# Kernel optimization log

Measured on AMD Instinct MI355X. Metric: run time of the kernel, lower is better.

The kernel has to match this reference:

```python
import jax, jax.numpy as jnp
import numpy as np


def setup_inputs() -> dict:
    key = jax.random.key(0)
    k1, k2 = jax.random.split(key)
    B, C, h, w = 8, 128, 56, 56
    query_feature = jax.random.normal(k1, (B, C, h, w), dtype=jnp.float32)
    support_feature = jax.random.normal(k2, (B, C, h, w), dtype=jnp.float32)
    return {"query_feature": query_feature, "support_feature": support_feature}


def reference(query_feature, support_feature):
    q, s = query_feature, support_feature
    B, C, h, w = support_feature.shape
    N = h * w
    # torch .view semantics == row-major reshape (NOT a transpose)
    qf = jnp.reshape(query_feature, (B, N, C))      # [B, N, C]
    sf = jnp.reshape(support_feature, (B, C, N))    # [B, C, N]
    batch_adj = jnp.einsum('bnc,bcm->bnm', qf, sf)  # [B, N, N]
    attn = jax.nn.softmax(batch_adj, axis=-1)
    query_logits = jnp.einsum('bnm,bmc->bnc', attn, qf)          # [B, N, C]
    attention_mask = jax.nn.sigmoid(jnp.sum(batch_adj, axis=-1)) # [B, N]
    query_logits = query_logits * attention_mask[..., None]
    sf2 = jnp.reshape(support_feature, (B, N, C))   # another raw view
    support_logits = sf2 * attention_mask[..., None]
    query_logits = jnp.reshape(query_logits, (B, C, h, w))
    support_logits = jnp.reshape(support_logits, (B, C, h, w))
    return (q + query_logits, s + support_logits)
```

## Files before the change

kernel.cpp:

```cpp
#include <hip/hip_runtime.h>
#include <math.h>

#define B_ 8
#define C_ 128
#define N_ 3136
#define MT 64
#define QTBIG 128
#define TILES 49
#define QTILES 25
#define SPLIT0 25

typedef short bf16x8 __attribute__((ext_vector_type(8)));
typedef float f32x4 __attribute__((ext_vector_type(4)));

__device__ __forceinline__ unsigned short f2bf(float f) {
    union { float f; unsigned u; } x; x.f = f;
    return (unsigned short)((x.u + 0x8000u) >> 16);
}

__device__ __forceinline__ void gl_lds16(const void* g, void* l) {
    __builtin_amdgcn_global_load_lds(
        (const __attribute__((address_space(1))) unsigned int*)g,
        (__attribute__((address_space(3))) unsigned int*)l, 16, 0, 0);
}

__global__ __launch_bounds__(256) void colsum_kernel(const float* __restrict__ s,
                                                     float* __restrict__ csum) {
    int blk = blockIdx.x;
    const float* p = s + (size_t)blk * N_;
    float acc = 0.f;
    for (int i = threadIdx.x; i < N_; i += 256) acc += p[i];
#pragma unroll
    for (int off = 32; off > 0; off >>= 1) acc += __shfl_down(acc, off, 64);
    __shared__ float part[4];
    if ((threadIdx.x & 63) == 0) part[threadIdx.x >> 6] = acc;
    __syncthreads();
    if (threadIdx.x == 0) csum[blk] = part[0] + part[1] + part[2] + part[3];
}

__global__ __launch_bounds__(256) void prep_kernel(const float* __restrict__ q,
                                                   const float* __restrict__ s,
                                                   unsigned short* __restrict__ sfT,
                                                   unsigned short* __restrict__ qfT) {
    __shared__ unsigned short T[8448];
    const int tid = threadIdx.x, bid = blockIdx.x;
    const int b = bid & 7, m0 = (bid >> 3) * 64;
    const float* sb = s + (size_t)b * C_ * N_;
    const float* qb = q + (size_t)b * C_ * N_;

    unsigned short (*TA)[132] = (unsigned short (*)[132])T;
#pragma unroll
    for (int st = 0; st < 8; ++st) {
        int idx = st * 256 + tid;
        int c = idx >> 4, m4 = (idx & 15) * 4;
        float4 v = *(const float4*)&sb[(size_t)c * N_ + m0 + m4];
        TA[m4 + 0][c] = f2bf(v.x);
        TA[m4 + 1][c] = f2bf(v.y);
        TA[m4 + 2][c] = f2bf(v.z);
        TA[m4 + 3][c] = f2bf(v.w);
    }
    __syncthreads();
    {
        unsigned short* dst = sfT + (size_t)b * N_ * C_;
#pragma unroll
        for (int st = 0; st < 4; ++st) {
            int g = st * 256 + tid;
            int mr = g >> 4, p = g & 15;
            int lch = p ^ (mr & 15);
            const unsigned short* src = &TA[mr][lch * 8];
            ushort4 a = *(const ushort4*)src;
            ushort4 bq = *(const ushort4*)(src + 4);
            uint4 w;
            w.x = a.x | ((unsigned)a.y << 16);   w.y = a.z | ((unsigned)a.w << 16);
            w.z = bq.x | ((unsigned)bq.y << 16); w.w = bq.z | ((unsigned)bq.w << 16);
            *(uint4*)&dst[(size_t)(m0 + mr) * C_ + p * 8] = w;
        }
    }
    __syncthreads();

    unsigned short (*TB)[66] = (unsigned short (*)[66])T;
#pragma unroll
    for (int st = 0; st < 8; ++st) {
        int idx = st * 256 + tid;
        int r = idx >> 5, c4 = (idx & 31) * 4;
        float4 v = *(const float4*)&qb[(size_t)(m0 + r) * C_ + c4];
        TB[c4 + 0][r] = f2bf(v.x);
        TB[c4 + 1][r] = f2bf(v.y);
        TB[c4 + 2][r] = f2bf(v.z);
        TB[c4 + 3][r] = f2bf(v.w);
    }
    __syncthreads();
    {
        unsigned short* dst = qfT + (size_t)b * C_ * N_;
#pragma unroll
        for (int st = 0; st < 4; ++st) {
            int g = st * 256 + tid;
            int c = g >> 3, p = g & 7;
            int lch = p ^ (c & 7);
            const unsigned short* src = &TB[c][lch * 8];
            ushort2 a0 = *(const ushort2*)(src);
            ushort2 a1 = *(const ushort2*)(src + 2);
            ushort2 a2 = *(const ushort2*)(src + 4);
            ushort2 a3 = *(const ushort2*)(src + 6);
            uint4 w;
            w.x = a0.x | ((unsigned)a0.y << 16); w.y = a1.x | ((unsigned)a1.y << 16);
            w.z = a2.x | ((unsigned)a2.y << 16); w.w = a3.x | ((unsigned)a3.y << 16);
            *(uint4*)&dst[(size_t)c * N_ + m0 + p * 8] = w;
        }
    }
}

__global__ __launch_bounds__(256, 2) void fused_split_kernel(
    const float* __restrict__ q,
    const unsigned short* __restrict__ sfT,
    const unsigned short* __restrict__ qfT,
    float* __restrict__ Opart, float* __restrict__ dpart) {

    __shared__ __align__(16) unsigned short Kb[2][MT * C_];
    __shared__ __align__(16) unsigned short Vb[2][C_ * MT];

    const int tid = threadIdx.x;
    const int lane = tid & 63;
    const int wave = tid >> 6;
    const int l15 = lane & 15;
    const int quad = lane >> 4;
    const int bid = blockIdx.x;
    const int b = bid & 7;
    const int rest = bid >> 3;
    const int qt = rest % QTILES;
    const int split = rest / QTILES;
    const int n0 = qt * QTBIG;
    const int t0 = split ? SPLIT0 : 0;
    const int t1 = split ? TILES : SPLIT0;

    const float* qb = q + (size_t)b * C_ * N_;
    const unsigned short* sfTb = sfT + (size_t)b * N_ * C_;
    const unsigned short* qfTb = qfT + (size_t)b * C_ * N_;

    const int sig_base = ((l15 >> 2) << 3) + (l15 & 3);

    {
        const size_t m1 = (size_t)t0 * MT;
#pragma unroll
        for (int st = 0; st < 4; ++st) {
            int i = st * 256 + tid;
            gl_lds16(sfTb + (m1 + (i >> 4)) * C_ + (i & 15) * 8,
                     &Kb[0][(st * 256 + wave * 64) * 8]);
            gl_lds16(qfTb + (size_t)(i >> 3) * N_ + m1 + (i & 7) * 8,
                     &Vb[0][(st * 256 + wave * 64) * 8]);
        }
    }

    bf16x8 qa[2][4];
#pragma unroll
    for (int rt = 0; rt < 2; ++rt) {
        int grow = n0 + wave * 32 + rt * 16 + l15;
        if (grow > N_ - 1) grow = N_ - 1;
#pragma unroll
        for (int ks = 0; ks < 4; ++ks) {
            int c0 = ks * 32 + quad * 8;
            float4 f0 = *(const float4*)&qb[(size_t)grow * C_ + c0];
            float4 f1 = *(const float4*)&qb[(size_t)grow * C_ + c0 + 4];
            union { unsigned short u[8]; bf16x8 v; } t;
            t.u[0] = f2bf(f0.x); t.u[1] = f2bf(f0.y);
            t.u[2] = f2bf(f0.z); t.u[3] = f2bf(f0.w);
            t.u[4] = f2bf(f1.x); t.u[5] = f2bf(f1.y);
            t.u[6] = f2bf(f1.z); t.u[7] = f2bf(f1.w);
            qa[rt][ks] = t.v;
        }
    }

    f32x4 O[2][8];
#pragma unroll
    for (int rt = 0; rt < 2; ++rt)
#pragma unroll
        for (int nt = 0; nt < 8; ++nt) O[rt][nt] = (f32x4){0.f, 0.f, 0.f, 0.f};
    float dsum[2] = {0.f, 0.f};

    const int ntiles = t1 - t0;
    for (int tt = 0; tt < ntiles; ++tt) {
        const int cur = tt & 1;
        __syncthreads();

        if (tt + 1 < ntiles) {
            const int nxt = cur ^ 1;
            const size_t m1 = (size_t)(t0 + tt + 1) * MT;
#pragma unroll
            for (int st = 0; st < 4; ++st) {
                int i = st * 256 + tid;
                gl_lds16(sfTb + (m1 + (i >> 4)) * C_ + (i & 15) * 8,
                         &Kb[nxt][(st * 256 + wave * 64) * 8]);
                gl_lds16(qfTb + (size_t)(i >> 3) * N_ + m1 + (i & 7) * 8,
                         &Vb[nxt][(st * 256 + wave * 64) * 8]);
            }
        }

        f32x4 acc[4][2];
#pragma unroll
        for (int ct = 0; ct < 4; ++ct) {
            acc[ct][0] = (f32x4){0.f, 0.f, 0.f, 0.f};
            acc[ct][1] = (f32x4){0.f, 0.f, 0.f, 0.f};
            const int mrow = sig_base + ((ct & 1) << 2) + ((ct >> 1) << 5);
#pragma unroll
            for (int ks = 0; ks < 4; ++ks) {
                int ch = (ks * 4 + quad) ^ (mrow & 15);
                bf16x8 af = *(const bf16x8*)&Kb[cur][mrow * C_ + ch * 8];
                acc[ct][0] = __builtin_amdgcn_mfma_f32_16x16x32_bf16(af, qa[0][ks], acc[ct][0], 0, 0, 0);
                acc[ct][1] = __builtin_amdgcn_mfma_f32_16x16x32_bf16(af, qa[1][ks], acc[ct][1], 0, 0, 0);
            }
        }

        bf16x8 pa[2][2];
#pragma unroll
        for (int k2 = 0; k2 < 2; ++k2)
#pragma unroll
            for (int rt = 0; rt < 2; ++rt) {
                float e0 = __expf(acc[2 * k2 + 0][rt][0]);
                float e1 = __expf(acc[2 * k2 + 0][rt][1]);
                float e2 = __expf(acc[2 * k2 + 0][rt][2]);
                float e3 = __expf(acc[2 * k2 + 0][rt][3]);
                float e4 = __expf(acc[2 * k2 + 1][rt][0]);
                float e5 = __expf(acc[2 * k2 + 1][rt][1]);
                float e6 = __expf(acc[2 * k2 + 1][rt][2]);
                float e7 = __expf(acc[2 * k2 + 1][rt][3]);
                dsum[rt] += ((e0 + e1) + (e2 + e3)) + ((e4 + e5) + (e6 + e7));
                union { unsigned short u[8]; bf16x8 v; } pk;
                pk.u[0] = f2bf(e0); pk.u[1] = f2bf(e1);
                pk.u[2] = f2bf(e2); pk.u[3] = f2bf(e3);
                pk.u[4] = f2bf(e4); pk.u[5] = f2bf(e5);
                pk.u[6] = f2bf(e6); pk.u[7] = f2bf(e7);
                pa[rt][k2] = pk.v;
            }

#pragma unroll
        for (int k2 = 0; k2 < 2; ++k2)
#pragma unroll
            for (int nt = 0; nt < 8; ++nt) {
                const int crow = nt * 16 + l15;
                int ch = (k2 * 4 + quad) ^ (crow & 7);
                bf16x8 vf = *(const bf16x8*)&Vb[cur][crow * MT + ch * 8];
                O[0][nt] = __builtin_amdgcn_mfma_f32_16x16x32_bf16(pa[0][k2], vf, O[0][nt], 0, 0, 0);
                O[1][nt] = __builtin_amdgcn_mfma_f32_16x16x32_bf16(pa[1][k2], vf, O[1][nt], 0, 0, 0);
            }
    }

#pragma unroll
    for (int rt = 0; rt < 2; ++rt) {
        float d = dsum[rt];
        d += __shfl_xor(d, 16, 64);
        d += __shfl_xor(d, 32, 64);
        if (quad == 0) {
            int grow = n0 + wave * 32 + rt * 16 + l15;
            if (grow < N_)
                dpart[(size_t)(split * 8 + b) * N_ + grow] = d;
        }
    }

#pragma unroll
    for (int rt = 0; rt < 2; ++rt)
#pragma unroll
        for (int r = 0; r < 4; ++r) {
            int grow = n0 + wave * 32 + rt * 16 + quad * 4 + r;
            if (grow < N_) {
                float* dst = Opart + ((size_t)(split * 8 + b) * N_ + grow) * C_;
#pragma unroll
                for (int nt = 0; nt < 8; ++nt)
                    dst[nt * 16 + l15] = O[rt][nt][r];
            }
        }
}

__global__ __launch_bounds__(256) void combine_kernel(
    const float* __restrict__ q, const float* __restrict__ s,
    const float* __restrict__ csum, const float* __restrict__ Opart,
    const float* __restrict__ dpart,
    float* __restrict__ out0, float* __restrict__ out1) {

    __shared__ float cs[C_];
    const int tid = threadIdx.x, bid = blockIdx.x;
    const int b = bid & 7, r0 = (bid >> 3) * 32;
    if (tid < C_) cs[tid] = csum[b * C_ + tid];
    __syncthreads();

    const int lane = tid & 63, wave = tid >> 6;
    const int row_l = wave * 8 + (lane >> 3);
    const int j = lane & 7;
    const int grow = r0 + row_l;
    const size_t base = (size_t)b * N_ * C_ + (size_t)grow * C_;

    float4 qv[4];
    float dot = 0.f;
#pragma unroll
    for (int k = 0; k < 4; ++k) {
        int c = k * 32 + j * 4;
        qv[k] = *(const float4*)&q[base + c];
        dot += qv[k].x * cs[c] + qv[k].y * cs[c + 1] +
               qv[k].z * cs[c + 2] + qv[k].w * cs[c + 3];
    }
    dot += __shfl_xor(dot, 1, 64);
    dot += __shfl_xor(dot, 2, 64);
    dot += __shfl_xor(dot, 4, 64);
    const float mask = 1.0f / (1.0f + __expf(-dot));

    const float dtot = dpart[(size_t)b * N_ + grow] +
                       dpart[(size_t)(8 + b) * N_ + grow];
    const float scl = mask / dtot;
    const float om = 1.0f + mask;

    const size_t p0 = ((size_t)b * N_ + grow) * C_;
    const size_t p1 = p0 + (size_t)8 * N_ * C_;
#pragma unroll
    for (int k = 0; k < 4; ++k) {
        int c = k * 32 + j * 4;
        float4 oa = *(const float4*)&Opart[p0 + c];
        float4 ob = *(const float4*)&Opart[p1 + c];
        float4 sv = *(const float4*)&s[base + c];
        float4 r0v, r1v;
        r0v.x = qv[k].x + (oa.x + ob.x) * scl;
        r0v.y = qv[k].y + (oa.y + ob.y) * scl;
        r0v.z = qv[k].z + (oa.z + ob.z) * scl;
        r0v.w = qv[k].w + (oa.w + ob.w) * scl;
        r1v.x = sv.x * om; r1v.y = sv.y * om;
        r1v.z = sv.z * om; r1v.w = sv.w * om;
        *(float4*)&out0[base + c] = r0v;
        *(float4*)&out1[base + c] = r1v;
    }
}

__global__ __launch_bounds__(256, 2) void fused_kernel(const float* __restrict__ q,
                                                       const float* __restrict__ s,
                                                       const float* __restrict__ csum,
                                                       float* __restrict__ out0,
                                                       float* __restrict__ out1) {
    __shared__ float QtT[C_][68];
    __shared__ float Kt[C_ * 32];
    __shared__ float Vt[32 * C_];
    __shared__ float PT[32][68];
    __shared__ float mask_l[64];
    __shared__ float csum_l[C_];

    const int t = threadIdx.x;
    const int l = t & 63, w = t >> 6, tx = t & 15, ty = t >> 4;
    const int bid = blockIdx.x, b = bid & 7, n0 = (bid >> 3) * 64;
    const float* qb = q + (size_t)b * C_ * N_;
    const float* sb = s + (size_t)b * C_ * N_;

#pragma unroll
    for (int jj = 0; jj < 2; ++jj) {
        int c = l + 64 * jj;
#pragma unroll
        for (int i = 0; i < 16; ++i) QtT[c][w + 4 * i] = qb[(size_t)(n0 + w + 4 * i) * C_ + c];
    }
    if (t < C_) csum_l[t] = csum[b * C_ + t];
    __syncthreads();
    if (t < 64) {
        float d = 0.f;
        for (int c = 0; c < C_; ++c) d += QtT[c][t] * csum_l[c];
        mask_l[t] = 1.0f / (1.0f + __expf(-d));
    }
    float4 Oa[4], Ob[4];
#pragma unroll
    for (int i = 0; i < 4; ++i) { Oa[i] = make_float4(0,0,0,0); Ob[i] = make_float4(0,0,0,0); }
    float m_r[4], l_r[4];
#pragma unroll
    for (int i = 0; i < 4; ++i) { m_r[i] = -3.0e38f; l_r[i] = 0.f; }

    for (int mt = 0; mt < N_ / 32; ++mt) {
        const int m0 = mt * 32;
        __syncthreads();
#pragma unroll
        for (int i = 0; i < 4; ++i) {
            int s4 = (w * 4 + i) * 64 + l;
            int c = s4 >> 3, mq = (s4 & 7) * 4;
            *(float4*)&Kt[c * 32 + mq] = *(const float4*)&sb[(size_t)c * N_ + m0 + mq];
            *(float4*)&Vt[s4 * 4] = *(const float4*)&qb[(size_t)m0 * C_ + s4 * 4];
        }
        __syncthreads();
        float a[4][2];
#pragma unroll
        for (int i = 0; i < 4; ++i) a[i][0] = a[i][1] = 0.f;
#pragma unroll 4
        for (int k = 0; k < C_; ++k) {
            const float4 qv = *(const float4*)&QtT[k][4 * ty];
            const float2 kv = *(const float2*)&Kt[k * 32 + 2 * tx];
            a[0][0] = fmaf(qv.x, kv.x, a[0][0]); a[0][1] = fmaf(qv.x, kv.y, a[0][1]);
            a[1][0] = fmaf(qv.y, kv.x, a[1][0]); a[1][1] = fmaf(qv.y, kv.y, a[1][1]);
            a[2][0] = fmaf(qv.z, kv.x, a[2][0]); a[2][1] = fmaf(qv.z, kv.y, a[2][1]);
            a[3][0] = fmaf(qv.w, kv.x, a[3][0]); a[3][1] = fmaf(qv.w, kv.y, a[3][1]);
        }
#pragma unroll
        for (int i = 0; i < 4; ++i) {
            float tm = fmaxf(a[i][0], a[i][1]);
            tm = fmaxf(tm, __shfl_xor(tm, 1, 64)); tm = fmaxf(tm, __shfl_xor(tm, 2, 64));
            tm = fmaxf(tm, __shfl_xor(tm, 4, 64)); tm = fmaxf(tm, __shfl_xor(tm, 8, 64));
            float nm = fmaxf(m_r[i], tm);
            float al = __expf(m_r[i] - nm);
            m_r[i] = nm;
            float p0 = __expf(a[i][0] - nm), p1 = __expf(a[i][1] - nm);
            float ts = p0 + p1;
            ts += __shfl_xor(ts, 1, 64); ts += __shfl_xor(ts, 2, 64);
            ts += __shfl_xor(ts, 4, 64); ts += __shfl_xor(ts, 8, 64);
            l_r[i] = l_r[i] * al + ts;
            PT[2 * tx + 0][4 * ty + i] = p0;
            PT[2 * tx + 1][4 * ty + i] = p1;
            Oa[i].x *= al; Oa[i].y *= al; Oa[i].z *= al; Oa[i].w *= al;
            Ob[i].x *= al; Ob[i].y *= al; Ob[i].z *= al; Ob[i].w *= al;
        }
        __syncthreads();
#pragma unroll 2
        for (int j = 0; j < 32; ++j) {
            const float4 pv = *(const float4*)&PT[j][4 * ty];
            const float4 v0 = *(const float4*)&Vt[j * C_ + 4 * tx];
            const float4 v1 = *(const float4*)&Vt[j * C_ + 4 * tx + 64];
            Oa[0].x = fmaf(pv.x, v0.x, Oa[0].x); Oa[0].y = fmaf(pv.x, v0.y, Oa[0].y);
            Oa[0].z = fmaf(pv.x, v0.z, Oa[0].z); Oa[0].w = fmaf(pv.x, v0.w, Oa[0].w);
            Ob[0].x = fmaf(pv.x, v1.x, Ob[0].x); Ob[0].y = fmaf(pv.x, v1.y, Ob[0].y);
            Ob[0].z = fmaf(pv.x, v1.z, Ob[0].z); Ob[0].w = fmaf(pv.x, v1.w, Ob[0].w);
            Oa[1].x = fmaf(pv.y, v0.x, Oa[1].x); Oa[1].y = fmaf(pv.y, v0.y, Oa[1].y);
            Oa[1].z = fmaf(pv.y, v0.z, Oa[1].z); Oa[1].w = fmaf(pv.y, v0.w, Oa[1].w);
            Ob[1].x = fmaf(pv.y, v1.x, Ob[1].x); Ob[1].y = fmaf(pv.y, v1.y, Ob[1].y);
            Ob[1].z = fmaf(pv.y, v1.z, Ob[1].z); Ob[1].w = fmaf(pv.y, v1.w, Ob[1].w);
            Oa[2].x = fmaf(pv.z, v0.x, Oa[2].x); Oa[2].y = fmaf(pv.z, v0.y, Oa[2].y);
            Oa[2].z = fmaf(pv.z, v0.z, Oa[2].z); Oa[2].w = fmaf(pv.z, v0.w, Oa[2].w);
            Ob[2].x = fmaf(pv.z, v1.x, Ob[2].x); Ob[2].y = fmaf(pv.z, v1.y, Ob[2].y);
            Ob[2].z = fmaf(pv.z, v1.z, Ob[2].z); Ob[2].w = fmaf(pv.z, v1.w, Ob[2].w);
            Oa[3].x = fmaf(pv.w, v0.x, Oa[3].x); Oa[3].y = fmaf(pv.w, v0.y, Oa[3].y);
            Oa[3].z = fmaf(pv.w, v0.z, Oa[3].z); Oa[3].w = fmaf(pv.w, v0.w, Oa[3].w);
            Ob[3].x = fmaf(pv.w, v1.x, Ob[3].x); Ob[3].y = fmaf(pv.w, v1.y, Ob[3].y);
            Ob[3].z = fmaf(pv.w, v1.z, Ob[3].z); Ob[3].w = fmaf(pv.w, v1.w, Ob[3].w);
        }
    }
#pragma unroll
    for (int i = 0; i < 4; ++i) {
        const int r = 4 * ty + i;
        const float mk = mask_l[r];
        const float scl = mk / l_r[i];
        const float om = 1.0f + mk;
        const size_t row = (size_t)b * C_ * N_ + (size_t)(n0 + r) * C_;
#pragma unroll
        for (int h = 0; h < 2; ++h) {
            const int c = 4 * tx + 64 * h;
            const float4 ov = h ? Ob[i] : Oa[i];
            float4 qv = *(const float4*)&qb[(size_t)(n0 + r) * C_ + c];
            float4 sv = *(const float4*)&sb[(size_t)(n0 + r) * C_ + c];
            float4 o0, o1;
            o0.x = qv.x + ov.x * scl; o0.y = qv.y + ov.y * scl;
            o0.z = qv.z + ov.z * scl; o0.w = qv.w + ov.w * scl;
            o1.x = sv.x * om; o1.y = sv.y * om; o1.z = sv.z * om; o1.w = sv.w * om;
            *(float4*)&out0[row + c] = o0;
            *(float4*)&out1[row + c] = o1;
        }
    }
}

extern "C" void kernel_launch(void* const* d_in, const int* in_sizes, int n_in,
                              void* d_out, int out_size, void* d_ws, size_t ws_size,
                              hipStream_t stream) {
    const float* q = (const float*)d_in[0];
    const float* s = (const float*)d_in[1];
    float* out0 = (float*)d_out;
    float* out1 = out0 + (size_t)B_ * C_ * N_;
    float* csum = (float*)d_ws;

    const size_t elems = (size_t)B_ * N_ * C_;
    const size_t need = 4096
                      + 2 * elems * sizeof(unsigned short)
                      + 2 * elems * sizeof(float)
                      + 2 * (size_t)B_ * N_ * sizeof(float);

    colsum_kernel<<<B_ * C_, 256, 0, stream>>>(s, csum);
    if (ws_size >= need) {
        unsigned short* sfT = (unsigned short*)((char*)d_ws + 4096);
        unsigned short* qfT = sfT + elems;
        float* Opart = (float*)(qfT + elems);
        float* dpart = Opart + 2 * elems;
        prep_kernel<<<B_ * TILES, 256, 0, stream>>>(q, s, sfT, qfT);
        fused_split_kernel<<<2 * QTILES * B_, 256, 0, stream>>>(q, sfT, qfT, Opart, dpart);
        combine_kernel<<<B_ * (N_ / 32), 256, 0, stream>>>(q, s, csum, Opart, dpart, out0, out1);
    } else {
        fused_kernel<<<B_ * (N_ / 64), 256, 0, stream>>>(q, s, csum, out0, out1);
    }
}
```

Measured before the change: 149.0 us.

## Split key range four ways, fuse colsum into prep, register-stage V buffer

Generalizes the key-dimension split from 2 to a runtime nsplit (4 when the workspace allows), giving 800 blocks instead of 400 for better CU fill. The separate colsum kernel is replaced by atomic partial sums inside prep_kernel after a memset. V is now single-buffered in LDS and prefetched through registers, which frees LDS so occupancy can rise to 3 blocks per SM. The costs are more partial-output traffic in the combine kernel, an extra barrier per tile, and float atomics that make the column sums nondeterministic in order.

After: 303.6 us. +103.7%, slower.

```diff
diff --git a/kernel.cpp b/kernel.cpp
--- a/kernel.cpp
+++ b/kernel.cpp
@@ -8,7 +8,6 @@
 #define QTBIG 128
 #define TILES 49
 #define QTILES 25
-#define SPLIT0 25
 
 typedef short bf16x8 __attribute__((ext_vector_type(8)));
 typedef float f32x4 __attribute__((ext_vector_type(4)));
@@ -41,7 +40,8 @@
 __global__ __launch_bounds__(256) void prep_kernel(const float* __restrict__ q,
                                                    const float* __restrict__ s,
                                                    unsigned short* __restrict__ sfT,
-                                                   unsigned short* __restrict__ qfT) {
+                                                   unsigned short* __restrict__ qfT,
+                                                   float* __restrict__ csum) {
     __shared__ unsigned short T[8448];
     const int tid = threadIdx.x, bid = blockIdx.x;
     const int b = bid & 7, m0 = (bid >> 3) * 64;
@@ -58,6 +58,12 @@
         TA[m4 + 1][c] = f2bf(v.y);
         TA[m4 + 2][c] = f2bf(v.z);
         TA[m4 + 3][c] = f2bf(v.w);
+        float part = v.x + v.y + v.z + v.w;
+        part += __shfl_xor(part, 1, 64);
+        part += __shfl_xor(part, 2, 64);
+        part += __shfl_xor(part, 4, 64);
+        part += __shfl_xor(part, 8, 64);
+        if ((tid & 15) == 0) atomicAdd(&csum[b * C_ + c], part);
     }
     __syncthreads();
     {
@@ -110,14 +116,15 @@
     }
 }
 
-__global__ __launch_bounds__(256, 2) void fused_split_kernel(
+__global__ __launch_bounds__(256, 3) void fused_split_kernel(
     const float* __restrict__ q,
     const unsigned short* __restrict__ sfT,
     const unsigned short* __restrict__ qfT,
-    float* __restrict__ Opart, float* __restrict__ dpart) {
+    float* __restrict__ Opart, float* __restrict__ dpart,
+    int nsplit) {
 
     __shared__ __align__(16) unsigned short Kb[2][MT * C_];
-    __shared__ __align__(16) unsigned short Vb[2][C_ * MT];
+    __shared__ __align__(16) unsigned short Vb[C_ * MT];
 
     const int tid = threadIdx.x;
     const int lane = tid & 63;
@@ -130,8 +137,9 @@
     const int qt = rest % QTILES;
     const int split = rest / QTILES;
     const int n0 = qt * QTBIG;
-    const int t0 = split ? SPLIT0 : 0;
-    const int t1 = split ? TILES : SPLIT0;
+    const int per = TILES / nsplit, rem = TILES % nsplit;
+    const int t0 = split * per + (split < rem ? split : rem);
+    const int ntiles = per + (split < rem ? 1 : 0);
 
     const float* qb = q + (size_t)b * C_ * N_;
     const unsigned short* sfTb = sfT + (size_t)b * N_ * C_;
@@ -147,7 +155,7 @@
             gl_lds16(sfTb + (m1 + (i >> 4)) * C_ + (i & 15) * 8,
                      &Kb[0][(st * 256 + wave * 64) * 8]);
             gl_lds16(qfTb + (size_t)(i >> 3) * N_ + m1 + (i & 7) * 8,
-                     &Vb[0][(st * 256 + wave * 64) * 8]);
+                     &Vb[(st * 256 + wave * 64) * 8]);
         }
     }
 
@@ -177,12 +185,12 @@
         for (int nt = 0; nt < 8; ++nt) O[rt][nt] = (f32x4){0.f, 0.f, 0.f, 0.f};
     float dsum[2] = {0.f, 0.f};
 
-    const int ntiles = t1 - t0;
     for (int tt = 0; tt < ntiles; ++tt) {
         const int cur = tt & 1;
+        const int more = (tt + 1 < ntiles);
         __syncthreads();
 
-        if (tt + 1 < ntiles) {
+        if (more) {
             const int nxt = cur ^ 1;
             const size_t m1 = (size_t)(t0 + tt + 1) * MT;
 #pragma unroll
@@ -190,8 +198,6 @@
                 int i = st * 256 + tid;
                 gl_lds16(sfTb + (m1 + (i >> 4)) * C_ + (i & 15) * 8,
                          &Kb[nxt][(st * 256 + wave * 64) * 8]);
-                gl_lds16(qfTb + (size_t)(i >> 3) * N_ + m1 + (i & 7) * 8,
-                         &Vb[nxt][(st * 256 + wave * 64) * 8]);
             }
         }
 
@@ -232,16 +238,35 @@
                 pa[rt][k2] = pk.v;
             }
 
+        uint4 vreg[4];
+        if (more) {
+            const size_t m1 = (size_t)(t0 + tt + 1) * MT;
+#pragma unroll
+            for (int j = 0; j < 4; ++j) {
+                int i = j * 256 + tid;
+                vreg[j] = *(const uint4*)(qfTb + (size_t)(i >> 3) * N_ + m1 + (i & 7) * 8);
+            }
+        }
+
 #pragma unroll
         for (int k2 = 0; k2 < 2; ++k2)
 #pragma unroll
             for (int nt = 0; nt < 8; ++nt) {
                 const int crow = nt * 16 + l15;
                 int ch = (k2 * 4 + quad) ^ (crow & 7);
-                bf16x8 vf = *(const bf16x8*)&Vb[cur][crow * MT + ch * 8];
+                bf16x8 vf = *(const bf16x8*)&Vb[crow * MT + ch * 8];
                 O[0][nt] = __builtin_amdgcn_mfma_f32_16x16x32_bf16(pa[0][k2], vf, O[0][nt], 0, 0, 0);
                 O[1][nt] = __builtin_amdgcn_mfma_f32_16x16x32_bf16(pa[1][k2], vf, O[1][nt], 0, 0, 0);
             }
+
+        if (more) {
+            __syncthreads();
+#pragma unroll
+            for (int j = 0; j < 4; ++j) {
+                int i = j * 256 + tid;
+                *(uint4*)&Vb[i * 8] = vreg[j];
+            }
+        }
     }
 
 #pragma unroll
@@ -274,7 +299,7 @@
     const float* __restrict__ q, const float* __restrict__ s,
     const float* __restrict__ csum, const float* __restrict__ Opart,
     const float* __restrict__ dpart,
-    float* __restrict__ out0, float* __restrict__ out1) {
+    float* __restrict__ out0, float* __restrict__ out1, int nsplit) {
 
     __shared__ float cs[C_];
     const int tid = threadIdx.x, bid = blockIdx.x;
@@ -302,24 +327,27 @@
     dot += __shfl_xor(dot, 4, 64);
     const float mask = 1.0f / (1.0f + __expf(-dot));
 
-    const float dtot = dpart[(size_t)b * N_ + grow] +
-                       dpart[(size_t)(8 + b) * N_ + grow];
+    float dtot = 0.f;
+    for (int sp = 0; sp < nsplit; ++sp)
+        dtot += dpart[(size_t)(sp * 8 + b) * N_ + grow];
     const float scl = mask / dtot;
     const float om = 1.0f + mask;
 
-    const size_t p0 = ((size_t)b * N_ + grow) * C_;
-    const size_t p1 = p0 + (size_t)8 * N_ * C_;
 #pragma unroll
     for (int k = 0; k < 4; ++k) {
         int c = k * 32 + j * 4;
-        float4 oa = *(const float4*)&Opart[p0 + c];
-        float4 ob = *(const float4*)&Opart[p1 + c];
+        float4 oa = make_float4(0.f, 0.f, 0.f, 0.f);
+        for (int sp = 0; sp < nsplit; ++sp) {
+            const size_t p = ((size_t)(sp * 8 + b) * N_ + grow) * C_;
+            float4 t = *(const float4*)&Opart[p + c];
+            oa.x += t.x; oa.y += t.y; oa.z += t.z; oa.w += t.w;
+        }
         float4 sv = *(const float4*)&s[base + c];
         float4 r0v, r1v;
-        r0v.x = qv[k].x + (oa.x + ob.x) * scl;
-        r0v.y = qv[k].y + (oa.y + ob.y) * scl;
-        r0v.z = qv[k].z + (oa.z + ob.z) * scl;
-        r0v.w = qv[k].w + (oa.w + ob.w) * scl;
+        r0v.x = qv[k].x + oa.x * scl;
+        r0v.y = qv[k].y + oa.y * scl;
+        r0v.z = qv[k].z + oa.z * scl;
+        r0v.w = qv[k].w + oa.w * scl;
         r1v.x = sv.x * om; r1v.y = sv.y * om;
         r1v.z = sv.z * om; r1v.w = sv.w * om;
         *(float4*)&out0[base + c] = r0v;
@@ -463,21 +491,30 @@
     float* csum = (float*)d_ws;
 
     const size_t elems = (size_t)B_ * N_ * C_;
-    const size_t need = 4096
-                      + 2 * elems * sizeof(unsigned short)
-                      + 2 * elems * sizeof(float)
-                      + 2 * (size_t)B_ * N_ * sizeof(float);
-
-    colsum_kernel<<<B_ * C_, 256, 0, stream>>>(s, csum);
-    if (ws_size >= need) {
+    auto need = [&](int ns) {
+        return (size_t)4096
+             + 2 * elems * sizeof(unsigned short)
+             + (size_t)ns * elems * sizeof(float)
+             + (size_t)ns * B_ * N_ * sizeof(float);
+    };
+
+    int ns = 0;
+    if (ws_size >= need(4)) ns = 4;
+    else if (ws_size >= need(2)) ns = 2;
+
+    if (ns > 0) {
         unsigned short* sfT = (unsigned short*)((char*)d_ws + 4096);
         unsigned short* qfT = sfT + elems;
         float* Opart = (float*)(qfT + elems);
-        float* dpart = Opart + 2 * elems;
-        prep_kernel<<<B_ * TILES, 256, 0, stream>>>(q, s, sfT, qfT);
-        fused_split_kernel<<<2 * QTILES * B_, 256, 0, stream>>>(q, sfT, qfT, Opart, dpart);
-        combine_kernel<<<B_ * (N_ / 32), 256, 0, stream>>>(q, s, csum, Opart, dpart, out0, out1);
+        float* dpart = Opart + (size_t)ns * elems;
+        hipMemsetAsync(csum, 0, B_ * C_ * sizeof(float), stream);
+        prep_kernel<<<B_ * TILES, 256, 0, stream>>>(q, s, sfT, qfT, csum);
+        fused_split_kernel<<<ns * QTILES * B_, 256, 0, stream>>>(
+            q, sfT, qfT, Opart, dpart, ns);
+        combine_kernel<<<B_ * (N_ / 32), 256, 0, stream>>>(q, s, csum, Opart, dpart,
+                                                           out0, out1, ns);
     } else {
+        colsum_kernel<<<B_ * C_, 256, 0, stream>>>(s, csum);
         fused_kernel<<<B_ * (N_ / 64), 256, 0, stream>>>(q, s, csum, out0, out1);
     }
 }
```
